# Optimization experiments

Measured on AMD Instinct MI355X. Metric: run time of the kernel, lower is better.

The kernel has to match this reference:

```python
import jax, jax.numpy as jnp
import numpy as np

N_V, MAXN = 20000, 16   # vertices, padded neighbors
C, N = 32, 8            # in_channels, regular-rep size
B = 8                   # basis size (circulant basis of C_N)


def setup_inputs() -> dict:
    key = jax.random.key(0)
    ks = jax.random.split(key, 13)
    inp = {
        "x": jax.random.normal(ks[0], (N_V, C, N), jnp.float32),
        "neighbors": jax.random.randint(ks[1], (N_V, MAXN), 0, N_V),
        "mask": jax.random.bernoulli(ks[2], 0.8, (N_V, MAXN)),
        "parallel_transport_matrices": jax.random.normal(ks[3], (N_V, MAXN, N, N), jnp.float32),
        "rel_pos_u": jax.random.normal(ks[4], (N_V, MAXN, 2), jnp.float32),
        # buffers (fixed bases)
        "reg_to_reg_basis": jax.random.normal(ks[5], (B, N, N), jnp.float32),
        "value_basis_zero": jax.random.normal(ks[6], (B, N, N), jnp.float32),
        "value_basis_first": jax.random.normal(ks[7], (B, 2, N, N), jnp.float32),
        "value_basis_second": jax.random.normal(ks[8], (B, 3, N, N), jnp.float32),
        # learned parameters
        "query_coeffs": 0.02 * jax.random.normal(ks[9], (C, B), jnp.float32),
        "key_coeffs": 0.02 * jax.random.normal(ks[10], (C, B), jnp.float32),
        "w0_params": 0.02 * jax.random.normal(ks[11], (C, B), jnp.float32),
        "w1_params": 0.02 * jax.random.normal(ks[12], (C, B), jnp.float32),
        "w2_params": 0.02 * jax.random.normal(jax.random.fold_in(key, 99), (C, B), jnp.float32),
    }
    return inp


def reference(x, neighbors, mask, parallel_transport_matrices, rel_pos_u,
              reg_to_reg_basis, value_basis_zero, value_basis_first, value_basis_second,
              query_coeffs, key_coeffs, w0_params, w1_params, w2_params):
    maskf = mask.astype(x.dtype)                               # [V, Mn]
    # gather neighbor features and zero out padding
    x_neigh = x[neighbors] * maskf[:, :, None, None]           # [V, Mn, C, N]
    # parallel transport each neighbor's feature
    f_prime = jnp.einsum('vnij,vncj->vnci', parallel_transport_matrices, x_neigh)
    # keys (center) and queries (transported neighbors)
    W_K = jnp.einsum('cb,bij->cij', key_coeffs, reg_to_reg_basis)
    K = jnp.einsum('cij,vcj->vi', W_K, x)                      # [V, N]
    W_Q = jnp.einsum('cb,bij->cij', query_coeffs, reg_to_reg_basis)
    Q = jnp.einsum('cij,vncj->vni', W_Q, f_prime)              # [V, Mn, N]
    # relu-mean attention score, masked and normalized
    score = jax.nn.relu(Q + K[:, None, :]).mean(axis=-1)       # [V, Mn]
    score = jnp.where(mask, score, 0.0)
    denom = jnp.clip(score.sum(axis=-1, keepdims=True), 1e-8)
    attention = score / denom                                  # [V, Mn]
    # polynomial value basis in rel-pos u
    u0, u1 = rel_pos_u[..., 0], rel_pos_u[..., 1]
    u_quad = jnp.stack([u0 * u0, 2.0 * u0 * u1, u1 * u1], axis=-1)  # [V, Mn, 3]
    W0 = jnp.einsum('cb,bij->cij', w0_params, value_basis_zero)
    values = jnp.einsum('cij,vncj->vnci', W0, f_prime)
    W1 = jnp.einsum('cb,boij->coij', w1_params, value_basis_first)
    values = values + jnp.einsum('coij,vno,vncj->vnci', W1, rel_pos_u, f_prime)
    W2 = jnp.einsum('cb,boij->coij', w2_params, value_basis_second)
    values = values + jnp.einsum('coij,vno,vncj->vnci', W2, u_quad, f_prime)
    # attention-weighted reduction over neighbors
    out = jnp.einsum('vn,vnci->vci', attention, values)        # [V, C, N]
    return out
```

## Files before the change

kernel.cpp:

```cpp
#include <hip/hip_runtime.h>

#define NV   20000
#define MAXN 16

__global__ void detect_mask_kind(const unsigned int* __restrict__ m,
                                 int* __restrict__ flag) {
    if (threadIdx.x == 0 && blockIdx.x == 0) {
        int allint = 1, allflt = 1;
        #pragma unroll 8
        for (int k = 0; k < 64; ++k) {
            unsigned w = m[k];
            if (!(w == 0u || w == 1u)) allint = 0;
            if (!(w == 0u || w == 0x3F800000u)) allflt = 0;
        }
        *flag = allint ? 0 : (allflt ? 2 : 1);
    }
}

__global__ void compute_weights(const float* __restrict__ rr,
                                const float* __restrict__ vb0,
                                const float* __restrict__ vb1,
                                const float* __restrict__ vb2,
                                const float* __restrict__ qc,
                                const float* __restrict__ kc,
                                const float* __restrict__ w0p,
                                const float* __restrict__ w1p,
                                const float* __restrict__ w2p,
                                float4* __restrict__ wt) {
    const int t = threadIdx.x;
    const int c = t & 31;
    const int i = t >> 5;
    float WQr[8], WKr[8], W0r[8], W1r0[8], W1r1[8], W2r0[8], W2r1[8], W2r2[8];
    #pragma unroll
    for (int j = 0; j < 8; ++j) {
        WQr[j] = 0.f; WKr[j] = 0.f; W0r[j] = 0.f; W1r0[j] = 0.f;
        W1r1[j] = 0.f; W2r0[j] = 0.f; W2r1[j] = 0.f; W2r2[j] = 0.f;
    }
    #pragma unroll
    for (int b = 0; b < 8; ++b) {
        const float qcb = qc[c * 8 + b];
        const float kcb = kc[c * 8 + b];
        const float w0b = w0p[c * 8 + b];
        const float w1b = w1p[c * 8 + b];
        const float w2b = w2p[c * 8 + b];
        const float* rrb = rr  + b * 64  + i * 8;
        const float* z0  = vb0 + b * 64  + i * 8;
        const float* z1  = vb1 + b * 128 + i * 8;
        const float* z2  = vb2 + b * 192 + i * 8;
        #pragma unroll
        for (int j = 0; j < 8; ++j) {
            const float r = rrb[j];
            WQr[j]  = fmaf(qcb, r, WQr[j]);
            WKr[j]  = fmaf(kcb, r, WKr[j]);
            W0r[j]  = fmaf(w0b, z0[j],       W0r[j]);
            W1r0[j] = fmaf(w1b, z1[j],       W1r0[j]);
            W1r1[j] = fmaf(w1b, z1[64 + j],  W1r1[j]);
            W2r0[j] = fmaf(w2b, z2[j],       W2r0[j]);
            W2r1[j] = fmaf(w2b, z2[64 + j],  W2r1[j]);
            W2r2[j] = fmaf(w2b, z2[128 + j], W2r2[j]);
        }
    }
    float4* o = wt + t * 16;
    o[ 0] = *(const float4*)&WQr[0];  o[ 1] = *(const float4*)&WQr[4];
    o[ 2] = *(const float4*)&WKr[0];  o[ 3] = *(const float4*)&WKr[4];
    o[ 4] = *(const float4*)&W0r[0];  o[ 5] = *(const float4*)&W0r[4];
    o[ 6] = *(const float4*)&W1r0[0]; o[ 7] = *(const float4*)&W1r0[4];
    o[ 8] = *(const float4*)&W1r1[0]; o[ 9] = *(const float4*)&W1r1[4];
    o[10] = *(const float4*)&W2r0[0]; o[11] = *(const float4*)&W2r0[4];
    o[12] = *(const float4*)&W2r1[0]; o[13] = *(const float4*)&W2r1[4];
    o[14] = *(const float4*)&W2r2[0]; o[15] = *(const float4*)&W2r2[4];
}

__device__ __forceinline__ float dot8a(const float* __restrict__ w,
                                       const float* __restrict__ f) {
    float s = w[0] * f[0];
    #pragma unroll
    for (int j = 1; j < 8; ++j) s = fmaf(w[j], f[j], s);
    return s;
}

__device__ __forceinline__ float dot8f4(const float4& a, const float4& b,
                                        const float* __restrict__ f) {
    return fmaf(a.x, f[0], fmaf(a.y, f[1], fmaf(a.z, f[2], fmaf(a.w, f[3],
           fmaf(b.x, f[4], fmaf(b.y, f[5], fmaf(b.z, f[6], b.w * f[7])))))));
}

__global__ void __launch_bounds__(256, 5)
ge_attn_kernel(const float* __restrict__ x,
               const int*   __restrict__ neighbors,
               const void*  __restrict__ maskp,
               const float* __restrict__ ptm,
               const float* __restrict__ rpu,
               const float4* __restrict__ wt,
               const int*   __restrict__ mflag,
               float*       __restrict__ out) {
    const int t = threadIdx.x;
    const int c = t & 31;
    const int i = t >> 5;
    const int mf = *mflag;

    __shared__ float fsh2[8][32][17];
    __shared__ float Fsh[8][32][6];
    __shared__ float sqni[16][8];
    __shared__ float kk[8];
    __shared__ float sn[16];
    __shared__ float smask[16];

    const int v  = blockIdx.x;
    const int vq = v * 16;

    if (t < 128) ((float*)sqni)[t] = 0.f;
    else if (t < 144) sn[t - 128] = 0.f;
    if (t < 16) {
        int mm;
        if (mf == 0)      mm = (((const int*)maskp)[vq + t] != 0);
        else if (mf == 1) mm = (((const unsigned char*)maskp)[vq + t] != 0);
        else              mm = (((const float*)maskp)[vq + t] != 0.0f);
        smask[t] = mm ? 1.f : 0.f;
    }

    float WQK[16];
    {
        const float4* wp = wt + t * 16;
        #pragma unroll
        for (int r = 0; r < 4; ++r) {
            const float4 q = wp[r];
            WQK[r * 4 + 0] = q.x; WQK[r * 4 + 1] = q.y;
            WQK[r * 4 + 2] = q.z; WQK[r * 4 + 3] = q.w;
        }
        #pragma unroll
        for (int r = 0; r < 16; ++r)
            asm volatile("" : "+v"(WQK[r]));
    }

    #pragma unroll
    for (int sub = 0; sub < 2; ++sub) {
        const int n = 2 * i + sub;
        int mm;
        if (mf == 0)      mm = (((const int*)maskp)[vq + n] != 0);
        else if (mf == 1) mm = (((const unsigned char*)maskp)[vq + n] != 0);
        else              mm = (((const float*)maskp)[vq + n] != 0.0f);
        const float m = mm ? 1.f : 0.f;
        const int nbv = neighbors[vq + n];
        float xn[8];
        {
            const float* xnp = x + (size_t)nbv * 256 + c * 8;
            *(float4*)&xn[0] = *(const float4*)xnp;
            *(float4*)&xn[4] = *(const float4*)(xnp + 4);
        }
        const float4* P4 = (const float4*)(ptm + (size_t)(vq + n) * 64);
        #pragma unroll
        for (int j2 = 0; j2 < 4; ++j2) {
            fsh2[2 * j2    ][c][n] = dot8f4(P4[4 * j2 + 0], P4[4 * j2 + 1], xn) * m;
            fsh2[2 * j2 + 1][c][n] = dot8f4(P4[4 * j2 + 2], P4[4 * j2 + 3], xn) * m;
        }
    }

    {
        float xc[8];
        const float* xv = x + (size_t)v * 256 + c * 8;
        *(float4*)&xc[0] = *(const float4*)xv;
        *(float4*)&xc[4] = *(const float4*)(xv + 4);
        float kp = dot8a(&WQK[8], xc);
        kp += __shfl_xor(kp, 1);
        kp += __shfl_xor(kp, 2);
        kp += __shfl_xor(kp, 4);
        kp += __shfl_xor(kp, 8);
        kp += __shfl_xor(kp, 16);
        if ((t & 31) == 0) kk[i] = kp;
    }

    __syncthreads();

    #pragma unroll 2
    for (int n2 = 0; n2 < 8; ++n2) {
        const int n = 2 * n2;
        float fa[8], fb[8];
        #pragma unroll
        for (int j = 0; j < 8; ++j) {
            fa[j] = fsh2[j][c][n];
            fb[j] = fsh2[j][c][n + 1];
        }
        float qa = dot8a(&WQK[0], fa);
        float qb = dot8a(&WQK[0], fb);
        qa += __shfl_xor(qa, 1);  qb += __shfl_xor(qb, 1);
        qa += __shfl_xor(qa, 2);  qb += __shfl_xor(qb, 2);
        qa += __shfl_xor(qa, 4);  qb += __shfl_xor(qb, 4);
        if ((c & 7) == 0) {
            atomicAdd(&sqni[n][i], qa);
            atomicAdd(&sqni[n + 1][i], qb);
        }
    }

    float WV[48];
    {
        const float4* wp = wt + t * 16 + 4;
        #pragma unroll
        for (int r = 0; r < 12; ++r) {
            const float4 q = wp[r];
            WV[r * 4 + 0] = q.x; WV[r * 4 + 1] = q.y;
            WV[r * 4 + 2] = q.z; WV[r * 4 + 3] = q.w;
        }
    }

    __syncthreads();

    if (t < 128) {
        const int nn = t >> 3, ii = t & 7;
        atomicAdd(&sn[nn], fmaxf(sqni[nn][ii] + kk[ii], 0.f));
    }

    __syncthreads();

    #pragma unroll
    for (int r = 0; r < 48; ++r)
        asm volatile("" : "+v"(WV[r]));

    float F0 = 0.f, F1 = 0.f, F2 = 0.f, F3 = 0.f, F4 = 0.f, F5 = 0.f;
    float ssum = 0.f;
    #pragma unroll 4
    for (int n2 = 0; n2 < 8; ++n2) {
        const int n = 2 * n2;
        const float sca = 0.125f * sn[n] * smask[n];
        const float scb = 0.125f * sn[n + 1] * smask[n + 1];
        const float u0a = rpu[(size_t)(vq + n) * 2];
        const float u1a = rpu[(size_t)(vq + n) * 2 + 1];
        const float u0b = rpu[(size_t)(vq + n + 1) * 2];
        const float u1b = rpu[(size_t)(vq + n + 1) * 2 + 1];
        const float fa = fsh2[i][c][n];
        const float fb = fsh2[i][c][n + 1];
        ssum += sca + scb;
        const float fsa = fa * sca;
        const float fsb = fb * scb;
        F0 += fsa + fsb;
        F1 = fmaf(u0a, fsa, fmaf(u0b, fsb, F1));
        F2 = fmaf(u1a, fsa, fmaf(u1b, fsb, F2));
        F3 = fmaf(u0a * u0a, fsa, fmaf(u0b * u0b, fsb, F3));
        F4 = fmaf(2.f * u0a * u1a, fsa, fmaf(2.f * u0b * u1b, fsb, F4));
        F5 = fmaf(u1a * u1a, fsa, fmaf(u1b * u1b, fsb, F5));
    }
    *(float2*)&Fsh[i][c][0] = make_float2(F0, F1);
    *(float2*)&Fsh[i][c][2] = make_float2(F2, F3);
    *(float2*)&Fsh[i][c][4] = make_float2(F4, F5);

    __syncthreads();

    float a0 = 0.f, a1 = 0.f, a2 = 0.f;
    #pragma unroll
    for (int jj = 0; jj < 8; ++jj) {
        const float2 F01 = *(const float2*)&Fsh[jj][c][0];
        const float2 F23 = *(const float2*)&Fsh[jj][c][2];
        const float2 F45 = *(const float2*)&Fsh[jj][c][4];
        a0 = fmaf(WV[     jj], F01.x, a0);
        a1 = fmaf(WV[ 8 + jj], F01.y, a1);
        a2 = fmaf(WV[16 + jj], F23.x, a2);
        a0 = fmaf(WV[24 + jj], F23.y, a0);
        a1 = fmaf(WV[32 + jj], F45.x, a1);
        a2 = fmaf(WV[40 + jj], F45.y, a2);
    }
    const float acc = a0 + a1 + a2;
    out[(size_t)v * 256 + c * 8 + i] = acc / fmaxf(ssum, 1e-8f);
}

extern "C" void kernel_launch(void* const* d_in, const int* in_sizes, int n_in,
                              void* d_out, int out_size, void* d_ws, size_t ws_size,
                              hipStream_t stream) {
    const float* x         = (const float*)d_in[0];
    const int*   neighbors = (const int*)d_in[1];
    const void*  maskp     = d_in[2];
    const float* ptm       = (const float*)d_in[3];
    const float* rpu       = (const float*)d_in[4];
    const float* rr        = (const float*)d_in[5];
    const float* vb0       = (const float*)d_in[6];
    const float* vb1       = (const float*)d_in[7];
    const float* vb2       = (const float*)d_in[8];
    const float* qc        = (const float*)d_in[9];
    const float* kc        = (const float*)d_in[10];
    const float* w0p       = (const float*)d_in[11];
    const float* w1p       = (const float*)d_in[12];
    const float* w2p       = (const float*)d_in[13];
    float* out = (float*)d_out;

    int*    flag = (int*)d_ws;
    float4* wtab = (float4*)((char*)d_ws + 1024);

    detect_mask_kind<<<1, 64, 0, stream>>>((const unsigned int*)maskp, flag);
    compute_weights<<<1, 256, 0, stream>>>(rr, vb0, vb1, vb2,
                                           qc, kc, w0p, w1p, w2p, wtab);
    ge_attn_kernel<<<NV, 256, 0, stream>>>(x, neighbors, maskp, ptm, rpu,
                                           wtab, flag, out);
}
```

Measured before the change: 291.5 us.

## Process four vertices per block and fuse query reduction with relu scoring

Each block now loops over four vertices, so the per-thread weight registers (WQK and WV) are loaded once and reused across vertices, and the grid shrinks to a quarter of the blocks. The query dot product is now reduced across all 32 lanes and the key is added in registers before the relu. This removes the sqni and kk shared arrays and one barrier per vertex. Shared-memory padding goes from 17 to 18 so neighbor pairs can be read as float2. The cost is a serial loop inside each block, with less parallelism across blocks to hide gather latency.

```diff
diff --git a/kernel.cpp b/kernel.cpp
--- a/kernel.cpp
+++ b/kernel.cpp
@@ -2,6 +2,8 @@
 
 #define NV   20000
 #define MAXN 16
+#define VPB  4
+#define NBLK 5000
 
 __global__ void detect_mask_kind(const unsigned int* __restrict__ m,
                                  int* __restrict__ flag) {
@@ -99,27 +101,12 @@
     const int i = t >> 5;
     const int mf = *mflag;
 
-    __shared__ float fsh2[8][32][17];
+    __shared__ float fsh2[8][32][18];
     __shared__ float Fsh[8][32][6];
-    __shared__ float sqni[16][8];
-    __shared__ float kk[8];
     __shared__ float sn[16];
     __shared__ float smask[16];
 
-    const int v  = blockIdx.x;
-    const int vq = v * 16;
-
-    if (t < 128) ((float*)sqni)[t] = 0.f;
-    else if (t < 144) sn[t - 128] = 0.f;
-    if (t < 16) {
-        int mm;
-        if (mf == 0)      mm = (((const int*)maskp)[vq + t] != 0);
-        else if (mf == 1) mm = (((const unsigned char*)maskp)[vq + t] != 0);
-        else              mm = (((const float*)maskp)[vq + t] != 0.0f);
-        smask[t] = mm ? 1.f : 0.f;
-    }
-
-    float WQK[16];
+    float WQK[16], WV[48];
     {
         const float4* wp = wt + t * 16;
         #pragma unroll
@@ -129,137 +116,143 @@
             WQK[r * 4 + 2] = q.z; WQK[r * 4 + 3] = q.w;
         }
         #pragma unroll
-        for (int r = 0; r < 16; ++r)
-            asm volatile("" : "+v"(WQK[r]));
-    }
-
-    #pragma unroll
-    for (int sub = 0; sub < 2; ++sub) {
-        const int n = 2 * i + sub;
-        int mm;
-        if (mf == 0)      mm = (((const int*)maskp)[vq + n] != 0);
-        else if (mf == 1) mm = (((const unsigned char*)maskp)[vq + n] != 0);
-        else              mm = (((const float*)maskp)[vq + n] != 0.0f);
-        const float m = mm ? 1.f : 0.f;
-        const int nbv = neighbors[vq + n];
-        float xn[8];
-        {
-            const float* xnp = x + (size_t)nbv * 256 + c * 8;
-            *(float4*)&xn[0] = *(const float4*)xnp;
-            *(float4*)&xn[4] = *(const float4*)(xnp + 4);
-        }
-        const float4* P4 = (const float4*)(ptm + (size_t)(vq + n) * 64);
-        #pragma unroll
-        for (int j2 = 0; j2 < 4; ++j2) {
-            fsh2[2 * j2    ][c][n] = dot8f4(P4[4 * j2 + 0], P4[4 * j2 + 1], xn) * m;
-            fsh2[2 * j2 + 1][c][n] = dot8f4(P4[4 * j2 + 2], P4[4 * j2 + 3], xn) * m;
-        }
-    }
-
-    {
-        float xc[8];
-        const float* xv = x + (size_t)v * 256 + c * 8;
-        *(float4*)&xc[0] = *(const float4*)xv;
-        *(float4*)&xc[4] = *(const float4*)(xv + 4);
-        float kp = dot8a(&WQK[8], xc);
-        kp += __shfl_xor(kp, 1);
-        kp += __shfl_xor(kp, 2);
-        kp += __shfl_xor(kp, 4);
-        kp += __shfl_xor(kp, 8);
-        kp += __shfl_xor(kp, 16);
-        if ((t & 31) == 0) kk[i] = kp;
-    }
-
-    __syncthreads();
-
-    #pragma unroll 2
-    for (int n2 = 0; n2 < 8; ++n2) {
-        const int n = 2 * n2;
-        float fa[8], fb[8];
-        #pragma unroll
-        for (int j = 0; j < 8; ++j) {
-            fa[j] = fsh2[j][c][n];
-            fb[j] = fsh2[j][c][n + 1];
-        }
-        float qa = dot8a(&WQK[0], fa);
-        float qb = dot8a(&WQK[0], fb);
-        qa += __shfl_xor(qa, 1);  qb += __shfl_xor(qb, 1);
-        qa += __shfl_xor(qa, 2);  qb += __shfl_xor(qb, 2);
-        qa += __shfl_xor(qa, 4);  qb += __shfl_xor(qb, 4);
-        if ((c & 7) == 0) {
-            atomicAdd(&sqni[n][i], qa);
-            atomicAdd(&sqni[n + 1][i], qb);
-        }
-    }
-
-    float WV[48];
-    {
-        const float4* wp = wt + t * 16 + 4;
-        #pragma unroll
         for (int r = 0; r < 12; ++r) {
-            const float4 q = wp[r];
+            const float4 q = wp[r + 4];
             WV[r * 4 + 0] = q.x; WV[r * 4 + 1] = q.y;
             WV[r * 4 + 2] = q.z; WV[r * 4 + 3] = q.w;
         }
-    }
-
-    __syncthreads();
-
-    if (t < 128) {
-        const int nn = t >> 3, ii = t & 7;
-        atomicAdd(&sn[nn], fmaxf(sqni[nn][ii] + kk[ii], 0.f));
-    }
-
-    __syncthreads();
-
-    #pragma unroll
-    for (int r = 0; r < 48; ++r)
-        asm volatile("" : "+v"(WV[r]));
-
-    float F0 = 0.f, F1 = 0.f, F2 = 0.f, F3 = 0.f, F4 = 0.f, F5 = 0.f;
-    float ssum = 0.f;
-    #pragma unroll 4
-    for (int n2 = 0; n2 < 8; ++n2) {
-        const int n = 2 * n2;
-        const float sca = 0.125f * sn[n] * smask[n];
-        const float scb = 0.125f * sn[n + 1] * smask[n + 1];
-        const float u0a = rpu[(size_t)(vq + n) * 2];
-        const float u1a = rpu[(size_t)(vq + n) * 2 + 1];
-        const float u0b = rpu[(size_t)(vq + n + 1) * 2];
-        const float u1b = rpu[(size_t)(vq + n + 1) * 2 + 1];
-        const float fa = fsh2[i][c][n];
-        const float fb = fsh2[i][c][n + 1];
-        ssum += sca + scb;
-        const float fsa = fa * sca;
-        const float fsb = fb * scb;
-        F0 += fsa + fsb;
-        F1 = fmaf(u0a, fsa, fmaf(u0b, fsb, F1));
-        F2 = fmaf(u1a, fsa, fmaf(u1b, fsb, F2));
-        F3 = fmaf(u0a * u0a, fsa, fmaf(u0b * u0b, fsb, F3));
-        F4 = fmaf(2.f * u0a * u1a, fsa, fmaf(2.f * u0b * u1b, fsb, F4));
-        F5 = fmaf(u1a * u1a, fsa, fmaf(u1b * u1b, fsb, F5));
-    }
-    *(float2*)&Fsh[i][c][0] = make_float2(F0, F1);
-    *(float2*)&Fsh[i][c][2] = make_float2(F2, F3);
-    *(float2*)&Fsh[i][c][4] = make_float2(F4, F5);
-
-    __syncthreads();
-
-    float a0 = 0.f, a1 = 0.f, a2 = 0.f;
-    #pragma unroll
-    for (int jj = 0; jj < 8; ++jj) {
-        const float2 F01 = *(const float2*)&Fsh[jj][c][0];
-        const float2 F23 = *(const float2*)&Fsh[jj][c][2];
-        const float2 F45 = *(const float2*)&Fsh[jj][c][4];
-        a0 = fmaf(WV[     jj], F01.x, a0);
-        a1 = fmaf(WV[ 8 + jj], F01.y, a1);
-        a2 = fmaf(WV[16 + jj], F23.x, a2);
-        a0 = fmaf(WV[24 + jj], F23.y, a0);
-        a1 = fmaf(WV[32 + jj], F45.x, a1);
-        a2 = fmaf(WV[40 + jj], F45.y, a2);
-    }
-    const float acc = a0 + a1 + a2;
-    out[(size_t)v * 256 + c * 8 + i] = acc / fmaxf(ssum, 1e-8f);
+        #pragma unroll
+        for (int r = 0; r < 16; ++r) asm volatile("" : "+v"(WQK[r]));
+        #pragma unroll
+        for (int r = 0; r < 48; ++r) asm volatile("" : "+v"(WV[r]));
+    }
+
+    for (int vi = 0; vi < VPB; ++vi) {
+        const int v  = blockIdx.x * VPB + vi;
+        const int vq = v * 16;
+
+        if (t < 16) {
+            int mm;
+            if (mf == 0)      mm = (((const int*)maskp)[vq + t] != 0);
+            else if (mf == 1) mm = (((const unsigned char*)maskp)[vq + t] != 0);
+            else              mm = (((const float*)maskp)[vq + t] != 0.0f);
+            smask[t] = mm ? 1.f : 0.f;
+        } else if (t < 32) {
+            sn[t - 16] = 0.f;
+        }
+
+        #pragma unroll
+        for (int sub = 0; sub < 2; ++sub) {
+            const int n = 2 * i + sub;
+            int mm;
+            if (mf == 0)      mm = (((const int*)maskp)[vq + n] != 0);
+            else if (mf == 1) mm = (((const unsigned char*)maskp)[vq + n] != 0);
+            else              mm = (((const float*)maskp)[vq + n] != 0.0f);
+            const float m = mm ? 1.f : 0.f;
+            const int nbv = neighbors[vq + n];
+            float xn[8];
+            {
+                const float* xnp = x + (size_t)nbv * 256 + c * 8;
+                *(float4*)&xn[0] = *(const float4*)xnp;
+                *(float4*)&xn[4] = *(const float4*)(xnp + 4);
+            }
+            const float4* P4 = (const float4*)(ptm + (size_t)(vq + n) * 64);
+            #pragma unroll
+            for (int j2 = 0; j2 < 4; ++j2) {
+                fsh2[2 * j2    ][c][n] = dot8f4(P4[4 * j2 + 0], P4[4 * j2 + 1], xn) * m;
+                fsh2[2 * j2 + 1][c][n] = dot8f4(P4[4 * j2 + 2], P4[4 * j2 + 3], xn) * m;
+            }
+        }
+
+        float kreg;
+        {
+            float xc[8];
+            const float* xv = x + (size_t)v * 256 + c * 8;
+            *(float4*)&xc[0] = *(const float4*)xv;
+            *(float4*)&xc[4] = *(const float4*)(xv + 4);
+            float kp = dot8a(&WQK[8], xc);
+            kp += __shfl_xor(kp, 1);
+            kp += __shfl_xor(kp, 2);
+            kp += __shfl_xor(kp, 4);
+            kp += __shfl_xor(kp, 8);
+            kp += __shfl_xor(kp, 16);
+            kreg = kp;
+        }
+
+        __syncthreads();
+
+        #pragma unroll
+        for (int n2 = 0; n2 < 8; ++n2) {
+            const int n = 2 * n2;
+            float2 fj[8];
+            #pragma unroll
+            for (int j = 0; j < 8; ++j)
+                fj[j] = *(const float2*)&fsh2[j][c][n];
+            float qa = fj[0].x * WQK[0];
+            float qb = fj[0].y * WQK[0];
+            #pragma unroll
+            for (int j = 1; j < 8; ++j) {
+                qa = fmaf(fj[j].x, WQK[j], qa);
+                qb = fmaf(fj[j].y, WQK[j], qb);
+            }
+            #pragma unroll
+            for (int d = 1; d <= 16; d <<= 1) {
+                qa += __shfl_xor(qa, d);
+                qb += __shfl_xor(qb, d);
+            }
+            const float ra = fmaxf(qa + kreg, 0.f);
+            const float rb = fmaxf(qb + kreg, 0.f);
+            if ((t & 31) == 0) {
+                atomicAdd(&sn[n], ra);
+                atomicAdd(&sn[n + 1], rb);
+            }
+        }
+
+        __syncthreads();
+
+        float F0 = 0.f, F1 = 0.f, F2 = 0.f, F3 = 0.f, F4 = 0.f, F5 = 0.f;
+        float ssum = 0.f;
+        #pragma unroll
+        for (int n2 = 0; n2 < 8; ++n2) {
+            const int n = 2 * n2;
+            const float sca = 0.125f * sn[n] * smask[n];
+            const float scb = 0.125f * sn[n + 1] * smask[n + 1];
+            const float u0a = rpu[(size_t)(vq + n) * 2];
+            const float u1a = rpu[(size_t)(vq + n) * 2 + 1];
+            const float u0b = rpu[(size_t)(vq + n + 1) * 2];
+            const float u1b = rpu[(size_t)(vq + n + 1) * 2 + 1];
+            const float2 fp = *(const float2*)&fsh2[i][c][n];
+            ssum += sca + scb;
+            const float fsa = fp.x * sca;
+            const float fsb = fp.y * scb;
+            F0 += fsa + fsb;
+            F1 = fmaf(u0a, fsa, fmaf(u0b, fsb, F1));
+            F2 = fmaf(u1a, fsa, fmaf(u1b, fsb, F2));
+            F3 = fmaf(u0a * u0a, fsa, fmaf(u0b * u0b, fsb, F3));
+            F4 = fmaf(2.f * u0a * u1a, fsa, fmaf(2.f * u0b * u1b, fsb, F4));
+            F5 = fmaf(u1a * u1a, fsa, fmaf(u1b * u1b, fsb, F5));
+        }
+        *(float2*)&Fsh[i][c][0] = make_float2(F0, F1);
+        *(float2*)&Fsh[i][c][2] = make_float2(F2, F3);
+        *(float2*)&Fsh[i][c][4] = make_float2(F4, F5);
+
+        __syncthreads();
+
+        float a0 = 0.f, a1 = 0.f, a2 = 0.f;
+        #pragma unroll
+        for (int jj = 0; jj < 8; ++jj) {
+            const float2 F01 = *(const float2*)&Fsh[jj][c][0];
+            const float2 F23 = *(const float2*)&Fsh[jj][c][2];
+            const float2 F45 = *(const float2*)&Fsh[jj][c][4];
+            a0 = fmaf(WV[     jj], F01.x, a0);
+            a1 = fmaf(WV[ 8 + jj], F01.y, a1);
+            a2 = fmaf(WV[16 + jj], F23.x, a2);
+            a0 = fmaf(WV[24 + jj], F23.y, a0);
+            a1 = fmaf(WV[32 + jj], F45.x, a1);
+            a2 = fmaf(WV[40 + jj], F45.y, a2);
+        }
+        out[(size_t)v * 256 + c * 8 + i] = (a0 + a1 + a2) / fmaxf(ssum, 1e-8f);
+    }
 }
 
 extern "C" void kernel_launch(void* const* d_in, const int* in_sizes, int n_in,
@@ -287,6 +280,6 @@
     detect_mask_kind<<<1, 64, 0, stream>>>((const unsigned int*)maskp, flag);
     compute_weights<<<1, 256, 0, stream>>>(rr, vb0, vb1, vb2,
                                            qc, kc, w0p, w1p, w2p, wtab);
-    ge_attn_kernel<<<NV, 256, 0, stream>>>(x, neighbors, maskp, ptm, rpu,
-                                           wtab, flag, out);
-}
+    ge_attn_kernel<<<NBLK, 256, 0, stream>>>(x, neighbors, maskp, ptm, rpu,
+                                             wtab, flag, out);
+}
```

Measured after the change: 327.1 us. 12.2% more time.
